# Optimization experiments

Measured on AMD Instinct MI355X. Metric: run time of the kernel, lower is better.

The kernel has to match this reference:

```python
import jax, jax.numpy as jnp
import numpy as np

HEADS = 8


def setup_inputs() -> dict:
    key = jax.random.key(0)
    k1, k2, k3, k4 = jax.random.split(key, 4)
    B, H, W, DIM = 8, 32, 32, 512
    x = jax.random.normal(k1, (B, H, W, DIM), dtype=jnp.float32)
    # torch nn.Linear weights: [out_features, in_features]
    s = 1.0 / np.sqrt(DIM)
    wq = jax.random.uniform(k2, (DIM, DIM), dtype=jnp.float32, minval=-s, maxval=s)
    wk = jax.random.uniform(k3, (DIM, DIM), dtype=jnp.float32, minval=-s, maxval=s)
    wv = jax.random.uniform(k4, (DIM, DIM), dtype=jnp.float32, minval=-s, maxval=s)
    return {"x": x, "wq": wq, "wk": wk, "wv": wv}


def reference(x, wq, wk, wv):
    # x: [b, H, W, dim]
    b, H, W, dim = x.shape
    n, d = HEADS, dim // HEADS
    scale = d ** (-0.5)
    # q/k/v projections (torch Linear: x @ W.T), split into heads
    q = (x @ wq.T).reshape(b, H, W, n, d)
    k = (x @ wk.T).reshape(b, H, W, n, d)
    v = (x @ wv.T).reshape(b, H, W, n, d)
    # per-pixel, per-head q.k dot product -> [b, n, H, W]
    # (original: einsum('bhwnd,bhwdn->bnhw', q, k.mT))
    weights = jnp.einsum('bhwnd,bhwnd->bnhw', q, k)
    # dropout (p=0.1) is identity in eval mode; then scale and softmax over W axis
    weights = jax.nn.softmax(weights * scale, axis=-1)
    # value combine: weights [b,n,h,w] x value [b,n,x,y,d] -> [b,n,h,w,x,y]
    v_p = jnp.transpose(v, (0, 3, 1, 2, 4))  # [b, n, H, W, d]
    attn = jnp.einsum('bnhw,bnxyd->bnhwxy', weights, v_p)
    return attn
```

## Files before the change

kernel.cpp:

```cpp
#include <hip/hip_runtime.h>
#include <hip/hip_bf16.h>

#define DIM 512
#define NH 8
#define DH 64
#define HW 1024
#define NPIX 8192

typedef __attribute__((ext_vector_type(8))) short s16x8;
typedef __attribute__((ext_vector_type(4))) float f32x4;

union B8 { s16x8 v; __hip_bfloat16 h[8]; };

__global__ __launch_bounds__(64) void k_wvsum(const float* __restrict__ wv,
                                              float* __restrict__ wvt) {
  const int n = blockIdx.x >> 3;
  const int c = (blockIdx.x & 7) * 64 + threadIdx.x;
  const float* base = wv + (size_t)n * DH * DIM + c;
  float acc = 0.f;
#pragma unroll 8
  for (int d = 0; d < DH; ++d) acc += base[(size_t)d * DIM];
  wvt[c * NH + n] = acc;
}

__global__ __launch_bounds__(256) void k_vsum(const float* __restrict__ x,
                                              const float* __restrict__ wvt,
                                              float* __restrict__ vs) {
  const int t = threadIdx.x, wave = t >> 6, lane = t & 63;
  const int p = blockIdx.x * 4 + wave;
  const float* xp = x + (size_t)p * DIM + lane * 8;
  const f32x4 x0 = *(const f32x4*)(xp);
  const f32x4 x1 = *(const f32x4*)(xp + 4);
  float xf[8];
#pragma unroll
  for (int j = 0; j < 4; ++j) { xf[j] = x0[j]; xf[4 + j] = x1[j]; }
  float acc[8] = {0.f,0.f,0.f,0.f,0.f,0.f,0.f,0.f};
  const float* wp = wvt + lane * 64;
#pragma unroll
  for (int cc = 0; cc < 8; ++cc) {
    const f32x4 a = *(const f32x4*)(wp + cc * 8);
    const f32x4 b = *(const f32x4*)(wp + cc * 8 + 4);
#pragma unroll
    for (int j = 0; j < 4; ++j) { acc[j] += xf[cc] * a[j]; acc[4 + j] += xf[cc] * b[j]; }
  }
#pragma unroll
  for (int off = 32; off >= 1; off >>= 1) {
#pragma unroll
    for (int j = 0; j < 8; ++j) acc[j] += __shfl_xor(acc[j], off, 64);
  }
  if (lane == 0) {
    const int b_ = p >> 10, xy = p & 1023;
#pragma unroll
    for (int j = 0; j < 8; ++j) vs[(size_t)(b_ * NH + j) * HW + xy] = acc[j];
  }
}

#define LDK 72
__global__ __launch_bounds__(256) void k_qk(const float* __restrict__ x,
                                            const float* __restrict__ wq,
                                            const float* __restrict__ wk,
                                            float* __restrict__ sw) {
  __shared__ __hip_bfloat16 xs[64 * LDK];
  __shared__ __hip_bfloat16 wqs[64 * LDK];
  __shared__ __hip_bfloat16 wks[64 * LDK];
  __shared__ float wraw[64];

  const int t = threadIdx.x;
  const int wave = t >> 6, lane = t & 63;
  const int lrow = lane & 15, quad = lane >> 4;
  const int pix0 = blockIdx.x * 64;
  const int head = blockIdx.y;

  const float* xg = x + (size_t)pix0 * DIM;
  const float* qg = wq + (size_t)head * DH * DIM;
  const float* kg = wk + (size_t)head * DH * DIM;

  f32x4 accq[4], acck[4];
#pragma unroll
  for (int s = 0; s < 4; ++s) { accq[s] = (f32x4)0.f; acck[s] = (f32x4)0.f; }

  for (int k0 = 0; k0 < DIM; k0 += 64) {
    __syncthreads();
#pragma unroll
    for (int i = 0; i < 2; ++i) {
      const int j = t + i * 256;
      const int row = j >> 3, col = j & 7;
      const size_t goff = (size_t)row * DIM + k0 + col * 8;
      const int loff = row * LDK + col * 8;
      B8 ux, uq, uk;
      {
        const f32x4 a = *(const f32x4*)(xg + goff);
        const f32x4 b = *(const f32x4*)(xg + goff + 4);
#pragma unroll
        for (int m = 0; m < 4; ++m) { ux.h[m] = __float2bfloat16(a[m]); ux.h[4 + m] = __float2bfloat16(b[m]); }
      }
      {
        const f32x4 a = *(const f32x4*)(qg + goff);
        const f32x4 b = *(const f32x4*)(qg + goff + 4);
#pragma unroll
        for (int m = 0; m < 4; ++m) { uq.h[m] = __float2bfloat16(a[m]); uq.h[4 + m] = __float2bfloat16(b[m]); }
      }
      {
        const f32x4 a = *(const f32x4*)(kg + goff);
        const f32x4 b = *(const f32x4*)(kg + goff + 4);
#pragma unroll
        for (int m = 0; m < 4; ++m) { uk.h[m] = __float2bfloat16(a[m]); uk.h[4 + m] = __float2bfloat16(b[m]); }
      }
      *(s16x8*)(xs + loff)  = ux.v;
      *(s16x8*)(wqs + loff) = uq.v;
      *(s16x8*)(wks + loff) = uk.v;
    }
    __syncthreads();
#pragma unroll
    for (int kk = 0; kk < 64; kk += 32) {
      const s16x8 a = *(const s16x8*)(xs + (wave * 16 + lrow) * LDK + kk + quad * 8);
#pragma unroll
      for (int s = 0; s < 4; ++s) {
        const s16x8 bq = *(const s16x8*)(wqs + (s * 16 + lrow) * LDK + kk + quad * 8);
        accq[s] = __builtin_amdgcn_mfma_f32_16x16x32_bf16(a, bq, accq[s], 0, 0, 0);
        const s16x8 bk = *(const s16x8*)(wks + (s * 16 + lrow) * LDK + kk + quad * 8);
        acck[s] = __builtin_amdgcn_mfma_f32_16x16x32_bf16(a, bk, acck[s], 0, 0, 0);
      }
    }
  }

#pragma unroll
  for (int r = 0; r < 4; ++r) {
    float pr = accq[0][r] * acck[0][r] + accq[1][r] * acck[1][r]
             + accq[2][r] * acck[2][r] + accq[3][r] * acck[3][r];
#pragma unroll
    for (int off = 1; off <= 8; off <<= 1) pr += __shfl_xor(pr, off, 64);
    if (lrow == 0) wraw[wave * 16 + quad * 4 + r] = pr * 0.125f;
  }
  __syncthreads();

  if (t < 64) {
    const float v = wraw[t];
    float m = v;
#pragma unroll
    for (int off = 1; off <= 16; off <<= 1) m = fmaxf(m, __shfl_xor(m, off, 64));
    const float e = __expf(v - m);
    float se = e;
#pragma unroll
    for (int off = 1; off <= 16; off <<= 1) se += __shfl_xor(se, off, 64);
    const int p = pix0 + t;
    const int b_ = p >> 10, hw = p & 1023;
    sw[(size_t)(b_ * NH + head) * HW + hw] = e / se;
  }
}

__global__ __launch_bounds__(256) void k_out(const float* __restrict__ sw,
                                             const float* __restrict__ vs,
                                             float* __restrict__ out) {
  __shared__ float swl[32];
  const int bn = blockIdx.y;
  const int row0 = blockIdx.x * 32;
  const int t = threadIdx.x;
  if (t < 32) swl[t] = sw[(size_t)bn * HW + row0 + t];
  __syncthreads();
  const f32x4 va = *(const f32x4*)(vs + (size_t)bn * HW + t * 4);
  float* op = out + (size_t)bn * HW * HW + (size_t)row0 * HW + t * 4;
#pragma unroll 4
  for (int r = 0; r < 32; ++r) {
    const float w = swl[r];
    f32x4 o;
#pragma unroll
    for (int j = 0; j < 4; ++j) o[j] = w * va[j];
    __builtin_nontemporal_store(o, (f32x4*)(op + (size_t)r * HW));
  }
}

extern "C" void kernel_launch(void* const* d_in, const int* in_sizes, int n_in,
                              void* d_out, int out_size, void* d_ws, size_t ws_size,
                              hipStream_t stream) {
  const float* x  = (const float*)d_in[0];
  const float* wq = (const float*)d_in[1];
  const float* wk = (const float*)d_in[2];
  const float* wv = (const float*)d_in[3];
  float* out = (float*)d_out;

  float* wvt = (float*)d_ws;
  float* vs  = wvt + 4096;
  float* sw  = vs + 65536;

  hipLaunchKernelGGL(k_wvsum, dim3(64), dim3(64), 0, stream, wv, wvt);
  hipLaunchKernelGGL(k_vsum, dim3(NPIX / 4), dim3(256), 0, stream, x, wvt, vs);
  hipLaunchKernelGGL(k_qk, dim3(128, NH), dim3(256), 0, stream, x, wq, wk, sw);
  hipLaunchKernelGGL(k_out, dim3(32, 64), dim3(256), 0, stream, sw, vs, out);
}
```

Measured before the change: 332.5 us.

## Pre-convert x and weights to bf16 and restructure QK kernel per-head waves

Adds a prep kernel that converts wq/wk to bf16 once (merged with the wv column-sum), and makes the vsum kernel also write a bf16 copy of x. The QK kernel then reads bf16 operands straight from global memory without LDS staging, with one block of 32 pixels covering all 8 heads (one wave per head). This removes the repeated fp32 loads and conversions of x, which the old kernel redid for every head. In exchange it adds extra global writes and reads of the bf16 copies, and the operand loads no longer go through shared memory.

```diff
diff --git a/kernel.cpp b/kernel.cpp
--- a/kernel.cpp
+++ b/kernel.cpp
@@ -12,28 +12,52 @@
 
 union B8 { s16x8 v; __hip_bfloat16 h[8]; };
 
-__global__ __launch_bounds__(64) void k_wvsum(const float* __restrict__ wv,
+__global__ __launch_bounds__(256) void k_prep(const float* __restrict__ wq,
+                                              const float* __restrict__ wk,
+                                              const float* __restrict__ wv,
+                                              short* __restrict__ wqb,
+                                              short* __restrict__ wkb,
                                               float* __restrict__ wvt) {
-  const int n = blockIdx.x >> 3;
-  const int c = (blockIdx.x & 7) * 64 + threadIdx.x;
-  const float* base = wv + (size_t)n * DH * DIM + c;
-  float acc = 0.f;
+  const int b = blockIdx.x, t = threadIdx.x;
+  if (b < 256) {
+    const int half = b >> 7;
+    const float* src = half ? wk : wq;
+    short* dst = half ? wkb : wqb;
+    const int idx = ((b & 127) * 256 + t) * 8;
+    const f32x4 a = *(const f32x4*)(src + idx);
+    const f32x4 c = *(const f32x4*)(src + idx + 4);
+    B8 u;
+#pragma unroll
+    for (int m = 0; m < 4; ++m) { u.h[m] = __float2bfloat16(a[m]); u.h[4 + m] = __float2bfloat16(c[m]); }
+    *(s16x8*)(dst + idx) = u.v;
+  } else {
+    const int i = b - 256;
+    const int n = t >> 5, c = i * 32 + (t & 31);
+    const float* base = wv + (size_t)n * DH * DIM + c;
+    float acc = 0.f;
 #pragma unroll 8
-  for (int d = 0; d < DH; ++d) acc += base[(size_t)d * DIM];
-  wvt[c * NH + n] = acc;
+    for (int d = 0; d < DH; ++d) acc += base[(size_t)d * DIM];
+    wvt[c * NH + n] = acc;
+  }
 }
 
-__global__ __launch_bounds__(256) void k_vsum(const float* __restrict__ x,
-                                              const float* __restrict__ wvt,
-                                              float* __restrict__ vs) {
+__global__ __launch_bounds__(256) void k_xv(const float* __restrict__ x,
+                                            const float* __restrict__ wvt,
+                                            short* __restrict__ xb,
+                                            float* __restrict__ vs) {
   const int t = threadIdx.x, wave = t >> 6, lane = t & 63;
   const int p = blockIdx.x * 4 + wave;
   const float* xp = x + (size_t)p * DIM + lane * 8;
   const f32x4 x0 = *(const f32x4*)(xp);
   const f32x4 x1 = *(const f32x4*)(xp + 4);
   float xf[8];
+  B8 u;
 #pragma unroll
-  for (int j = 0; j < 4; ++j) { xf[j] = x0[j]; xf[4 + j] = x1[j]; }
+  for (int j = 0; j < 4; ++j) {
+    xf[j] = x0[j]; xf[4 + j] = x1[j];
+    u.h[j] = __float2bfloat16(x0[j]); u.h[4 + j] = __float2bfloat16(x1[j]);
+  }
+  *(s16x8*)(xb + (size_t)p * DIM + lane * 8) = u.v;
   float acc[8] = {0.f,0.f,0.f,0.f,0.f,0.f,0.f,0.f};
   const float* wp = wvt + lane * 64;
 #pragma unroll
@@ -55,95 +79,68 @@
   }
 }
 
-#define LDK 72
-__global__ __launch_bounds__(256) void k_qk(const float* __restrict__ x,
-                                            const float* __restrict__ wq,
-                                            const float* __restrict__ wk,
+__global__ __launch_bounds__(512) void k_qk(const short* __restrict__ xb,
+                                            const short* __restrict__ wqb,
+                                            const short* __restrict__ wkb,
                                             float* __restrict__ sw) {
-  __shared__ __hip_bfloat16 xs[64 * LDK];
-  __shared__ __hip_bfloat16 wqs[64 * LDK];
-  __shared__ __hip_bfloat16 wks[64 * LDK];
-  __shared__ float wraw[64];
+  __shared__ float sm[NH * 32];
+  const int t = threadIdx.x;
+  const int head = t >> 6, lane = t & 63;
+  const int lrow = lane & 15, quad = lane >> 4;
+  const int pix0 = blockIdx.x * 32;
 
-  const int t = threadIdx.x;
-  const int wave = t >> 6, lane = t & 63;
-  const int lrow = lane & 15, quad = lane >> 4;
-  const int pix0 = blockIdx.x * 64;
-  const int head = blockIdx.y;
+  const short* xr0 = xb + (size_t)(pix0 + lrow) * DIM + quad * 8;
+  const short* xr1 = xr0 + 16 * DIM;
+  const short* qb = wqb + (size_t)(head * DH + lrow) * DIM + quad * 8;
+  const short* kb = wkb + (size_t)(head * DH + lrow) * DIM + quad * 8;
 
-  const float* xg = x + (size_t)pix0 * DIM;
-  const float* qg = wq + (size_t)head * DH * DIM;
-  const float* kg = wk + (size_t)head * DH * DIM;
+  f32x4 accq[2][4], acck[2][4];
+#pragma unroll
+  for (int s = 0; s < 2; ++s)
+#pragma unroll
+    for (int o = 0; o < 4; ++o) { accq[s][o] = (f32x4)0.f; acck[s][o] = (f32x4)0.f; }
 
-  f32x4 accq[4], acck[4];
+#pragma unroll 2
+  for (int ks = 0; ks < 16; ++ks) {
+    const int off = ks * 32;
+    const s16x8 a0 = *(const s16x8*)(xr0 + off);
+    const s16x8 a1 = *(const s16x8*)(xr1 + off);
 #pragma unroll
-  for (int s = 0; s < 4; ++s) { accq[s] = (f32x4)0.f; acck[s] = (f32x4)0.f; }
-
-  for (int k0 = 0; k0 < DIM; k0 += 64) {
-    __syncthreads();
-#pragma unroll
-    for (int i = 0; i < 2; ++i) {
-      const int j = t + i * 256;
-      const int row = j >> 3, col = j & 7;
-      const size_t goff = (size_t)row * DIM + k0 + col * 8;
-      const int loff = row * LDK + col * 8;
-      B8 ux, uq, uk;
-      {
-        const f32x4 a = *(const f32x4*)(xg + goff);
-        const f32x4 b = *(const f32x4*)(xg + goff + 4);
-#pragma unroll
-        for (int m = 0; m < 4; ++m) { ux.h[m] = __float2bfloat16(a[m]); ux.h[4 + m] = __float2bfloat16(b[m]); }
-      }
-      {
-        const f32x4 a = *(const f32x4*)(qg + goff);
-        const f32x4 b = *(const f32x4*)(qg + goff + 4);
-#pragma unroll
-        for (int m = 0; m < 4; ++m) { uq.h[m] = __float2bfloat16(a[m]); uq.h[4 + m] = __float2bfloat16(b[m]); }
-      }
-      {
-        const f32x4 a = *(const f32x4*)(kg + goff);
-        const f32x4 b = *(const f32x4*)(kg + goff + 4);
-#pragma unroll
-        for (int m = 0; m < 4; ++m) { uk.h[m] = __float2bfloat16(a[m]); uk.h[4 + m] = __float2bfloat16(b[m]); }
-      }
-      *(s16x8*)(xs + loff)  = ux.v;
-      *(s16x8*)(wqs + loff) = uq.v;
-      *(s16x8*)(wks + loff) = uk.v;
-    }
-    __syncthreads();
-#pragma unroll
-    for (int kk = 0; kk < 64; kk += 32) {
-      const s16x8 a = *(const s16x8*)(xs + (wave * 16 + lrow) * LDK + kk + quad * 8);
-#pragma unroll
-      for (int s = 0; s < 4; ++s) {
-        const s16x8 bq = *(const s16x8*)(wqs + (s * 16 + lrow) * LDK + kk + quad * 8);
-        accq[s] = __builtin_amdgcn_mfma_f32_16x16x32_bf16(a, bq, accq[s], 0, 0, 0);
-        const s16x8 bk = *(const s16x8*)(wks + (s * 16 + lrow) * LDK + kk + quad * 8);
-        acck[s] = __builtin_amdgcn_mfma_f32_16x16x32_bf16(a, bk, acck[s], 0, 0, 0);
-      }
+    for (int o = 0; o < 4; ++o) {
+      const s16x8 bq = *(const s16x8*)(qb + o * 16 * DIM + off);
+      accq[0][o] = __builtin_amdgcn_mfma_f32_16x16x32_bf16(a0, bq, accq[0][o], 0, 0, 0);
+      accq[1][o] = __builtin_amdgcn_mfma_f32_16x16x32_bf16(a1, bq, accq[1][o], 0, 0, 0);
+      const s16x8 bk = *(const s16x8*)(kb + o * 16 * DIM + off);
+      acck[0][o] = __builtin_amdgcn_mfma_f32_16x16x32_bf16(a0, bk, acck[0][o], 0, 0, 0);
+      acck[1][o] = __builtin_amdgcn_mfma_f32_16x16x32_bf16(a1, bk, acck[1][o], 0, 0, 0);
     }
   }
 
 #pragma unroll
-  for (int r = 0; r < 4; ++r) {
-    float pr = accq[0][r] * acck[0][r] + accq[1][r] * acck[1][r]
-             + accq[2][r] * acck[2][r] + accq[3][r] * acck[3][r];
+  for (int s = 0; s < 2; ++s) {
 #pragma unroll
-    for (int off = 1; off <= 8; off <<= 1) pr += __shfl_xor(pr, off, 64);
-    if (lrow == 0) wraw[wave * 16 + quad * 4 + r] = pr * 0.125f;
+    for (int j = 0; j < 4; ++j) {
+      float pr = accq[s][0][j] * acck[s][0][j] + accq[s][1][j] * acck[s][1][j]
+               + accq[s][2][j] * acck[s][2][j] + accq[s][3][j] * acck[s][3][j];
+      pr += __shfl_xor(pr, 1, 64);
+      pr += __shfl_xor(pr, 2, 64);
+      pr += __shfl_xor(pr, 4, 64);
+      pr += __shfl_xor(pr, 8, 64);
+      if (lrow == 0) sm[head * 32 + s * 16 + quad * 4 + j] = pr * 0.125f;
+    }
   }
   __syncthreads();
 
-  if (t < 64) {
-    const float v = wraw[t];
-    float m = v;
+  const float v = sm[head * 32 + (lane & 31)];
+  float m = v;
 #pragma unroll
-    for (int off = 1; off <= 16; off <<= 1) m = fmaxf(m, __shfl_xor(m, off, 64));
-    const float e = __expf(v - m);
-    float se = e;
+  for (int off = 1; off <= 16; off <<= 1) m = fmaxf(m, __shfl_xor(m, off, 64));
+  const float e = __expf(v - m);
+  float se = e;
 #pragma unroll
-    for (int off = 1; off <= 16; off <<= 1) se += __shfl_xor(se, off, 64);
-    const int p = pix0 + t;
+  for (int off = 1; off <= 16; off <<= 1) se += __shfl_xor(se, off, 64);
+  if (lane < 32) {
+    const int p = pix0 + lane;
     const int b_ = p >> 10, hw = p & 1023;
     sw[(size_t)(b_ * NH + head) * HW + hw] = e / se;
   }
@@ -182,9 +179,12 @@
   float* wvt = (float*)d_ws;
   float* vs  = wvt + 4096;
   float* sw  = vs + 65536;
+  short* xb  = (short*)(sw + 65536);
+  short* wqb = xb + (size_t)NPIX * DIM;
+  short* wkb = wqb + DIM * DIM;
 
-  hipLaunchKernelGGL(k_wvsum, dim3(64), dim3(64), 0, stream, wv, wvt);
-  hipLaunchKernelGGL(k_vsum, dim3(NPIX / 4), dim3(256), 0, stream, x, wvt, vs);
-  hipLaunchKernelGGL(k_qk, dim3(128, NH), dim3(256), 0, stream, x, wq, wk, sw);
+  hipLaunchKernelGGL(k_prep, dim3(272), dim3(256), 0, stream, wq, wk, wv, wqb, wkb, wvt);
+  hipLaunchKernelGGL(k_xv, dim3(NPIX / 4), dim3(256), 0, stream, x, wvt, xb, vs);
+  hipLaunchKernelGGL(k_qk, dim3(NPIX / 32), dim3(512), 0, stream, xb, wqb, wkb, sw);
   hipLaunchKernelGGL(k_out, dim3(32, 64), dim3(256), 0, stream, sw, vs, out);
 }
```

Measured after the change: 344.3 us. +3.5%, slower.
